# Kernel tuning notes

Hardware: AMD Instinct MI355X
Metric: run time of the kernel (lower is better)

The kernel has to match this reference:

```python
import jax, jax.numpy as jnp
import numpy as np

EPS = 1e-12

def gcn_layer(x, W, row, col, vals, n_nodes):
    # support = x @ W ; out = relu(spmm(adj, support)) with adj in COO form
    support = x @ W                                  # [N, out]
    msgs = vals[:, None] * support[col]              # [E, out] gather
    agg = jax.ops.segment_sum(msgs, row, num_segments=n_nodes)
    return jax.nn.relu(agg)

def l2norm(x):
    return x / jnp.maximum(jnp.linalg.norm(x, axis=1, keepdims=True), EPS)

def setup_inputs() -> dict:
    key = jax.random.key(0)
    ks = jax.random.split(key, 16)
    N, D, A, Da, E = 20000, 1000, 1000, 100, 160000
    inp = {
        'emb_sr': jax.random.normal(ks[0], (N, D), jnp.float32) * 0.02,
        'emb_tg': jax.random.normal(ks[1], (N, D), jnp.float32) * 0.02,
        'attr_weight_sr': jax.random.uniform(ks[2], (N, A), jnp.float32),
        'attr_weight_tg': jax.random.uniform(ks[3], (N, A), jnp.float32),
        'row_sr': jax.random.randint(ks[4], (E,), 0, N, jnp.int32),
        'col_sr': jax.random.randint(ks[5], (E,), 0, N, jnp.int32),
        'vals_sr': jax.random.uniform(ks[6], (E,), jnp.float32),
        'row_tg': jax.random.randint(ks[7], (E,), 0, N, jnp.int32),
        'col_tg': jax.random.randint(ks[8], (E,), 0, N, jnp.int32),
        'vals_tg': jax.random.uniform(ks[9], (E,), jnp.float32),
        'W_s0': jax.random.normal(ks[10], (D, D), jnp.float32) * (1.0 / np.sqrt(D)),
        'W_s1': jax.random.normal(ks[11], (D, D), jnp.float32) * (1.0 / np.sqrt(D)),
        'W_a11': jax.random.normal(ks[12], (A, Da), jnp.float32) * (1.0 / np.sqrt(A)),
        'W_a12': jax.random.normal(ks[13], (A, Da), jnp.float32) * (1.0 / np.sqrt(A)),
        'W_a2': jax.random.normal(ks[14], (Da, Da), jnp.float32) * (1.0 / np.sqrt(Da)),
    }
    return inp

def reference(emb_sr, emb_tg, attr_weight_sr, attr_weight_tg,
              row_sr, col_sr, vals_sr, row_tg, col_tg, vals_tg,
              W_s0, W_s1, W_a11, W_a12, W_a2):
    N = emb_sr.shape[0]
    M = emb_tg.shape[0]
    # structural branch: 2 shared GCN layers over each graph
    sr = emb_sr
    tg = emb_tg
    for W in (W_s0, W_s1):
        sr = gcn_layer(sr, W, row_sr, col_sr, vals_sr, N)
        tg = gcn_layer(tg, W, row_tg, col_tg, vals_tg, M)
    sr = l2norm(sr)
    tg = l2norm(tg)
    # attribute branch
    sr_a = gcn_layer(attr_weight_sr, W_a11, row_sr, col_sr, vals_sr, N)
    sr_a = gcn_layer(sr_a, W_a2, row_sr, col_sr, vals_sr, N)
    tg_a = gcn_layer(attr_weight_tg, W_a12, row_tg, col_tg, vals_tg, M)
    tg_a = gcn_layer(tg_a, W_a2, row_tg, col_tg, vals_tg, M)
    return (sr, tg, sr_a, tg_a)
```

## Files before the change

kernel.cpp:

```cpp
#include <hip/hip_runtime.h>

#define N_NODES 20000
#define D_IN    1000
#define E_EDGES 160000
#define DA      100

#define MP   20096
#define DP   1024
#define DAP  128
#define MBLK 157
#define NRB  1250
#define PEMAX (E_EDGES + 4 * N_NODES)

typedef __bf16 bf16x8 __attribute__((ext_vector_type(8)));
typedef float  f32x4  __attribute__((ext_vector_type(4)));
typedef short  short8v __attribute__((ext_vector_type(8)));

__device__ __forceinline__ short f2bf(float f) {
  __bf16 h = (__bf16)f;
  return *(short*)&h;
}
__device__ __forceinline__ float bf2f(short s) {
  return __uint_as_float(((unsigned)(unsigned short)s) << 16);
}

#define GLDS16(g, l) __builtin_amdgcn_global_load_lds( \
    (const __attribute__((address_space(1))) void*)(g), \
    (__attribute__((address_space(3))) void*)(l), 16, 0, 0)


__global__ void cvt_pad2_k(const float* __restrict__ s0, const float* __restrict__ s1,
                           int R, int C,
                           short* __restrict__ d0, short* __restrict__ d1, int Cp) {
  const float* src = blockIdx.z ? s1 : s0;
  short* dst = blockIdx.z ? d1 : d0;
  int r = blockIdx.y;
  int c0 = threadIdx.x * 4;
  short4 o = {0, 0, 0, 0};
  if (r < R) {
    if (c0 + 3 < C) {
      float4 v = *(const float4*)&src[(size_t)r * C + c0];
      o.x = f2bf(v.x); o.y = f2bf(v.y); o.z = f2bf(v.z); o.w = f2bf(v.w);
    } else {
#pragma unroll
      for (int j = 0; j < 4; ++j) {
        float v = (c0 + j < C) ? src[(size_t)r * C + c0 + j] : 0.f;
        ((short*)&o)[j] = f2bf(v);
      }
    }
  }
  *(short4*)&dst[(size_t)r * Cp + c0] = o;
}

__global__ void cvt_w_t2_k(const float* __restrict__ s0, const float* __restrict__ s1,
                           int K, int Nc,
                           short* __restrict__ d0, short* __restrict__ d1, int Kp) {
  const float* src = blockIdx.z ? s1 : s0;
  short* dst = blockIdx.z ? d1 : d0;
  int n = blockIdx.y;
  int k = blockIdx.x * blockDim.x + threadIdx.x;
  if (k >= Kp) return;
  float v = (k < K && n < Nc) ? src[(size_t)k * Nc + n] : 0.f;
  dst[(size_t)n * Kp + k] = f2bf(v);
}

__global__ void zero_int_k(int* p, int n) {
  int i = blockIdx.x * blockDim.x + threadIdx.x;
  if (i < n) p[i] = 0;
}


__global__ void hist2_k(const int* __restrict__ row0, const int* __restrict__ row1, int E,
                        int* __restrict__ deg0, int* __restrict__ deg1) {
  int e = blockIdx.x * blockDim.x + threadIdx.x;
  if (e < E) atomicAdd(&deg0[row0[e]], 1);
  else if (e < 2 * E) atomicAdd(&deg1[row1[e - E]], 1);
}

#define SCAN_T 1024
#define SCAN_C 20
__launch_bounds__(SCAN_T)
__global__ void scan_pad2_k(const int* __restrict__ dg0, const int* __restrict__ dg1, int n,
                            int* __restrict__ p0, int* __restrict__ p1) {
  const int* deg = blockIdx.x ? dg1 : dg0;
  int* poffs = blockIdx.x ? p1 : p0;
  __shared__ int lds[SCAN_T];
  int t = threadIdx.x;
  int base = t * SCAN_C;
  int v[SCAN_C];
  int s = 0;
#pragma unroll
  for (int i = 0; i < SCAN_C; ++i) {
    int idx = base + i;
    int x = (idx < n) ? ((deg[idx] + 3) & ~3) : 0;
    s += x;
    v[i] = s;
  }
  lds[t] = s;
  __syncthreads();
  for (int off = 1; off < SCAN_T; off <<= 1) {
    int add = (t >= off) ? lds[t - off] : 0;
    __syncthreads();
    lds[t] += add;
    __syncthreads();
  }
  int prefix = lds[t] - s;
#pragma unroll
  for (int i = 0; i < SCAN_C; ++i) {
    int idx = base + i;
    if (idx < n) poffs[idx + 1] = v[i] + prefix;
  }
  if (t == 0) poffs[0] = 0;
}

__global__ void scatter_pack2_k(const int* __restrict__ row0, const int* __restrict__ col0,
                                const float* __restrict__ val0,
                                const int* __restrict__ row1, const int* __restrict__ col1,
                                const float* __restrict__ val1, int E,
                                const int* __restrict__ po0, const int* __restrict__ po1,
                                int* __restrict__ cur0, int* __restrict__ cur1,
                                int2* __restrict__ pk0, int2* __restrict__ pk1) {
  int e = blockIdx.x * blockDim.x + threadIdx.x;
  if (e < E) {
    int r = row0[e];
    int p = atomicAdd(&cur0[r], 1);
    pk0[po0[r] + p] = make_int2(col0[e], __float_as_int(val0[e]));
  } else if (e < 2 * E) {
    int ee = e - E;
    int r = row1[ee];
    int p = atomicAdd(&cur1[r], 1);
    pk1[po1[r] + p] = make_int2(col1[ee], __float_as_int(val1[ee]));
  }
}

__launch_bounds__(256, 2)
__global__ void gemm_bf16_k(const short* __restrict__ A0, const short* __restrict__ A1, int lda,
                            const short* __restrict__ Bt0, const short* __restrict__ Bt1, int ldb,
                            short* __restrict__ C0, short* __restrict__ C1, int ldc, int K,
                            int nbCol, int nbRow) {
  __shared__ short As[128 * 64];
  __shared__ short Bs[128 * 64];

  int orig = blockIdx.x;
  int nwg = gridDim.x;
  int q = nwg >> 3, rr = nwg & 7;
  int xcd = orig & 7, idx = orig >> 3;
  int wg = (xcd < rr ? xcd * (q + 1) : rr * (q + 1) + (xcd - rr) * q) + idx;
  int colB = wg % nbCol;
  int t2   = wg / nbCol;
  int rowB = t2 % nbRow;
  int z    = t2 / nbRow;

  const short* A  = z ? A1 : A0;
  const short* Bt = z ? Bt1 : Bt0;
  short* C        = z ? C1 : C0;

  const int tid  = threadIdx.x;
  const int lane = tid & 63;
  const int wid  = tid >> 6;
  const int wr   = wid >> 1;
  const int wc   = wid & 1;
  const int rowBase = rowB * 128;
  const int colBase = colB * 128;

  const int lrow = lane >> 3;
  const int kofs = (lane & 7) * 8;

  f32x4 acc[4][4];
#pragma unroll
  for (int m = 0; m < 4; ++m)
#pragma unroll
    for (int n = 0; n < 4; ++n)
      acc[m][n] = (f32x4){0.f, 0.f, 0.f, 0.f};

  for (int k0 = 0; k0 < K; k0 += 64) {
#pragma unroll
    for (int c = 0; c < 4; ++c) {
      int chunk = wid * 4 + c;
      int r = chunk * 8 + lrow;
      const short* g = A + (size_t)(rowBase + r) * lda + k0 + kofs;
      GLDS16(g, &As[chunk * 8 * 64]);
    }
#pragma unroll
    for (int c = 0; c < 4; ++c) {
      int chunk = wid * 4 + c;
      int r = chunk * 8 + lrow;
      const short* g = Bt + (size_t)(colBase + r) * ldb + k0 + kofs;
      GLDS16(g, &Bs[chunk * 8 * 64]);
    }
    __syncthreads();

    bf16x8 af[2][4], bfr[2][4];
#pragma unroll
    for (int kk = 0; kk < 2; ++kk) {
#pragma unroll
      for (int i = 0; i < 4; ++i) {
        int ar = wr * 64 + i * 16 + (lane & 15);
        af[kk][i]  = *(const bf16x8*)&As[ar * 64 + kk * 32 + (lane >> 4) * 8];
        int br = wc * 64 + i * 16 + (lane & 15);
        bfr[kk][i] = *(const bf16x8*)&Bs[br * 64 + kk * 32 + (lane >> 4) * 8];
      }
    }
#pragma unroll
    for (int kk = 0; kk < 2; ++kk)
#pragma unroll
      for (int m = 0; m < 4; ++m)
#pragma unroll
        for (int n = 0; n < 4; ++n)
          acc[m][n] = __builtin_amdgcn_mfma_f32_16x16x32_bf16(
              af[kk][m], bfr[kk][n], acc[m][n], 0, 0, 0);
    __syncthreads();
  }

#pragma unroll
  for (int m = 0; m < 4; ++m) {
#pragma unroll
    for (int n = 0; n < 4; ++n) {
      int row0 = rowBase + wr * 64 + m * 16 + (lane >> 4) * 4;
      int col  = colBase + wc * 64 + n * 16 + (lane & 15);
#pragma unroll
      for (int reg = 0; reg < 4; ++reg)
        C[(size_t)(row0 + reg) * ldc + col] = f2bf(acc[m][n][reg]);
    }
  }
}

template<int NCHUNK, int MODE>
__launch_bounds__(256)
__global__ void spmm_v5(const int* __restrict__ po0, const int* __restrict__ po1,
                        const int2* __restrict__ pk0, const int2* __restrict__ pk1,
                        const short* __restrict__ S0, const short* __restrict__ S1, int ldS,
                        short* __restrict__ oB0, short* __restrict__ oB1, int ldB,
                        float* __restrict__ oF0, float* __restrict__ oF1, int outCols) {
  int orig = blockIdx.x;
  int chunk, graph, rowBlk;
  if (NCHUNK == 8) {
    chunk = orig & 7;
    int idx = orig >> 3;
    graph = idx / NRB;
    rowBlk = idx - graph * NRB;
  } else {
    chunk = 0;
    graph = orig / NRB;
    rowBlk = orig - graph * NRB;
  }
  const int* poffs   = graph ? po1 : po0;
  const int2* packed = graph ? pk1 : pk0;
  const short* S     = graph ? S1 : S0;
  short* outB        = graph ? oB1 : oB0;
  float* outF        = graph ? oF1 : oF0;

  const int lane16 = threadIdx.x & 15;
  const int rowloc = threadIdx.x >> 4;
  const int r  = rowBlk * 16 + rowloc;
  const int c0 = chunk * 128 + lane16 * 8;

  int e0 = poffs[r], e1 = poffs[r + 1];
  float acc[8];
#pragma unroll
  for (int j = 0; j < 8; ++j) acc[j] = 0.f;

  for (int i = e0; i < e1; i += 4) {
    const int4* p4 = (const int4*)&packed[i];
    int4 a = p4[0];
    int4 b = p4[1];
    short8v s0 = *(const short8v*)&S[(size_t)a.x * ldS + c0];
    short8v s1 = *(const short8v*)&S[(size_t)a.z * ldS + c0];
    short8v s2 = *(const short8v*)&S[(size_t)b.x * ldS + c0];
    short8v s3 = *(const short8v*)&S[(size_t)b.z * ldS + c0];
    float v0 = __int_as_float(a.y);
    float v1 = __int_as_float(a.w);
    float v2 = __int_as_float(b.y);
    float v3 = __int_as_float(b.w);
#pragma unroll
    for (int j = 0; j < 8; ++j) {
      acc[j] += v0 * bf2f(s0[j]);
      acc[j] += v1 * bf2f(s1[j]);
      acc[j] += v2 * bf2f(s2[j]);
      acc[j] += v3 * bf2f(s3[j]);
    }
  }
#pragma unroll
  for (int j = 0; j < 8; ++j) acc[j] = fmaxf(acc[j], 0.f);

  if (MODE == 0) {
    short8v o;
#pragma unroll
    for (int j = 0; j < 8; ++j) o[j] = f2bf(acc[j]);
    *(short8v*)&outB[(size_t)r * ldB + c0] = o;
  } else {
#pragma unroll
    for (int j = 0; j < 8; ++j)
      if (c0 + j < outCols)
        outF[(size_t)r * outCols + c0 + j] = acc[j];
  }
}

__global__ void l2norm2_k(const short* __restrict__ H0, const short* __restrict__ H1, int ldH,
                          float* __restrict__ o0, float* __restrict__ o1, int cols) {
  const short* H = blockIdx.y ? H1 : H0;
  float* out = blockIdx.y ? o1 : o0;
  __shared__ float red[4];
  int r = blockIdx.x;
  int t = threadIdx.x;
  float s = 0.f;
  for (int c = t; c < ldH; c += 256) {
    float v = bf2f(H[(size_t)r * ldH + c]);
    s += v * v;
  }
  for (int off = 32; off >= 1; off >>= 1) s += __shfl_down(s, off, 64);
  if ((t & 63) == 0) red[t >> 6] = s;
  __syncthreads();
  float tot = red[0] + red[1] + red[2] + red[3];
  float inv = 1.f / fmaxf(sqrtf(tot), 1e-12f);
  for (int c = t; c < cols; c += 256)
    out[(size_t)r * cols + c] = bf2f(H[(size_t)r * ldH + c]) * inv;
}


extern "C" void kernel_launch(void* const* d_in, const int* in_sizes, int n_in,
                              void* d_out, int out_size, void* d_ws, size_t ws_size,
                              hipStream_t stream) {
  const float* emb_sr  = (const float*)d_in[0];
  const float* emb_tg  = (const float*)d_in[1];
  const float* attr_sr = (const float*)d_in[2];
  const float* attr_tg = (const float*)d_in[3];
  const int*   row_sr  = (const int*)d_in[4];
  const int*   col_sr  = (const int*)d_in[5];
  const float* vals_sr = (const float*)d_in[6];
  const int*   row_tg  = (const int*)d_in[7];
  const int*   col_tg  = (const int*)d_in[8];
  const float* vals_tg = (const float*)d_in[9];
  const float* W_s0    = (const float*)d_in[10];
  const float* W_s1    = (const float*)d_in[11];
  const float* W_a11   = (const float*)d_in[12];
  const float* W_a12   = (const float*)d_in[13];
  const float* W_a2    = (const float*)d_in[14];

  const int N = N_NODES, Dd = D_IN, E = E_EDGES;

  char* ws = (char*)d_ws;
  size_t off = 0;
  auto alloc = [&](size_t bytes) -> void* {
    void* p = ws + off;
    off += (bytes + 255) & ~(size_t)255;
    return p;
  };
  short* X0 = (short*)alloc((size_t)MP * DP * 2);
  short* X1 = (short*)alloc((size_t)MP * DP * 2);
  short* T0 = (short*)alloc((size_t)MP * DP * 2);
  short* T1 = (short*)alloc((size_t)MP * DP * 2);
  short* Ws0t  = (short*)alloc((size_t)DP * DP * 2);
  short* Ws1t  = (short*)alloc((size_t)DP * DP * 2);
  short* Wa11t = (short*)alloc((size_t)DAP * DP * 2);
  short* Wa12t = (short*)alloc((size_t)DAP * DP * 2);
  short* Wa2t  = (short*)alloc((size_t)DAP * DAP * 2);
  int*  ibuf    = (int*)alloc((size_t)4 * N * 4);
  int2* pack_sr = (int2*)alloc((size_t)PEMAX * 8);
  int2* pack_tg = (int2*)alloc((size_t)PEMAX * 8);
  int*  poffs_sr = (int*)alloc((size_t)(N + 1) * 4);
  int*  poffs_tg = (int*)alloc((size_t)(N + 1) * 4);
  if (off > ws_size) return;

  int* deg_sr = ibuf;
  int* cur_sr = ibuf + N;
  int* deg_tg = ibuf + 2 * N;
  int* cur_tg = ibuf + 3 * N;
  const int ZERO_N = 4 * N + 2 * (PEMAX * 2);

  float* out_sr  = (float*)d_out;
  float* out_tg  = out_sr + (size_t)N * Dd;
  float* out_sra = out_tg + (size_t)N * Dd;
  float* out_tga = out_sra + (size_t)N * DA;

  zero_int_k<<<dim3((ZERO_N + 255) / 256), 256, 0, stream>>>(ibuf, ZERO_N);
  hist2_k<<<dim3((2 * E + 255) / 256), 256, 0, stream>>>(row_sr, row_tg, E, deg_sr, deg_tg);
  scan_pad2_k<<<2, SCAN_T, 0, stream>>>(deg_sr, deg_tg, N, poffs_sr, poffs_tg);
  scatter_pack2_k<<<dim3((2 * E + 255) / 256), 256, 0, stream>>>(
      row_sr, col_sr, vals_sr, row_tg, col_tg, vals_tg, E,
      poffs_sr, poffs_tg, cur_sr, cur_tg, pack_sr, pack_tg);

  cvt_w_t2_k<<<dim3(DP / 256, DP, 2), 256, 0, stream>>>(W_s0, W_s1, Dd, Dd, Ws0t, Ws1t, DP);
  cvt_w_t2_k<<<dim3(DP / 256, DAP, 2), 256, 0, stream>>>(W_a11, W_a12, Dd, DA, Wa11t, Wa12t, DP);
  cvt_w_t2_k<<<dim3(1, DAP, 1), 256, 0, stream>>>(W_a2, W_a2, DA, DA, Wa2t, Wa2t, DAP);

  cvt_pad2_k<<<dim3(1, MP, 2), 256, 0, stream>>>(emb_sr, emb_tg, N, Dd, X0, X1, DP);
  gemm_bf16_k<<<dim3(8 * MBLK * 2), 256, 0, stream>>>(X0, X1, DP, Ws0t, Ws0t, DP,
                                                      T0, T1, DP, DP, 8, MBLK);
  spmm_v5<8, 0><<<dim3(8 * 2 * NRB), 256, 0, stream>>>(
      poffs_sr, poffs_tg, pack_sr, pack_tg, T0, T1, DP, X0, X1, DP, nullptr, nullptr, 0);
  gemm_bf16_k<<<dim3(8 * MBLK * 2), 256, 0, stream>>>(X0, X1, DP, Ws1t, Ws1t, DP,
                                                      T0, T1, DP, DP, 8, MBLK);
  spmm_v5<8, 0><<<dim3(8 * 2 * NRB), 256, 0, stream>>>(
      poffs_sr, poffs_tg, pack_sr, pack_tg, T0, T1, DP, X0, X1, DP, nullptr, nullptr, 0);
  l2norm2_k<<<dim3(N, 2), 256, 0, stream>>>(X0, X1, DP, out_sr, out_tg, Dd);

  cvt_pad2_k<<<dim3(1, MP, 2), 256, 0, stream>>>(attr_sr, attr_tg, N, Dd, X0, X1, DP);
  gemm_bf16_k<<<dim3(1 * MBLK * 2), 256, 0, stream>>>(X0, X1, DP, Wa11t, Wa12t, DP,
                                                      T0, T1, DAP, DP, 1, MBLK);
  spmm_v5<1, 0><<<dim3(2 * NRB), 256, 0, stream>>>(
      poffs_sr, poffs_tg, pack_sr, pack_tg, T0, T1, DAP, X0, X1, DAP, nullptr, nullptr, 0);
  gemm_bf16_k<<<dim3(1 * MBLK * 2), 256, 0, stream>>>(X0, X1, DAP, Wa2t, Wa2t, DAP,
                                                      T0, T1, DAP, DAP, 1, MBLK);
  spmm_v5<1, 1><<<dim3(2 * NRB), 256, 0, stream>>>(
      poffs_sr, poffs_tg, pack_sr, pack_tg, T0, T1, DAP, nullptr, nullptr, 0, out_sra, out_tga, DA);
}
```

Measured before the change: 636.2 us.

## Add 4-stage pipelined 128x256 bf16 GEMM for structural layers

Introduces a new GEMM kernel with 512 threads, 128x256 output tiles, and a four-buffer LDS ring. It uses direct global-to-LDS loads issued three k-steps ahead, with waitcnt-based synchronization and MFMA priority raising. It replaces the older 128x128 GEMM for the two large 1024-wide structural layers. The goal is to hide global memory latency and raise tile reuse, at the cost of more LDS, one block per CU, and hand-tuned waitcnt counts that must match the load count.

```diff
diff --git a/kernel.cpp b/kernel.cpp
--- a/kernel.cpp
+++ b/kernel.cpp
@@ -130,6 +130,119 @@
     int r = row1[ee];
     int p = atomicAdd(&cur1[r], 1);
     pk1[po1[r] + p] = make_int2(col1[ee], __float_as_int(val1[ee]));
+  }
+}
+
+template<int NT>
+__launch_bounds__(512, 1)
+__global__ void gemm_pipe_k(const short* __restrict__ A0, const short* __restrict__ A1, int lda,
+                            const short* __restrict__ Bt0, const short* __restrict__ Bt1, int ldb,
+                            short* __restrict__ C0, short* __restrict__ C1, int ldc,
+                            int nbCol, int nbRow) {
+  __shared__ short As[4][128 * 32];
+  __shared__ short Bs[4][256 * 32];
+
+  int orig = blockIdx.x;
+  int nwg = gridDim.x;
+  int q = nwg >> 3, rr = nwg & 7;
+  int xcd = orig & 7, idx = orig >> 3;
+  int wg = (xcd < rr ? xcd * (q + 1) : rr * (q + 1) + (xcd - rr) * q) + idx;
+  int colB = wg % nbCol;
+  int t2 = wg / nbCol;
+  int rowB = t2 % nbRow;
+  int z = t2 / nbRow;
+
+  const short* A  = z ? A1 : A0;
+  const short* Bt = z ? Bt1 : Bt0;
+  short* C        = z ? C1 : C0;
+
+  const int tid  = threadIdx.x;
+  const int lane = tid & 63;
+  const int wid  = tid >> 6;
+  const int wm   = wid >> 2;
+  const int wn   = wid & 3;
+  const int rowBase = rowB * 128;
+  const int colBase = colB * 256;
+
+  const int sRow   = tid >> 2;
+  const int sChunk = (tid & 3) ^ ((tid >> 3) & 3);
+  const short* gA  = A  + (size_t)(rowBase + sRow) * lda + sChunk * 8;
+  const short* gB0 = Bt + (size_t)(colBase + sRow) * ldb + sChunk * 8;
+  const short* gB1 = Bt + (size_t)(colBase + 128 + sRow) * ldb + sChunk * 8;
+  const int ldsA  = wid * 512;
+  const int ldsB0 = wid * 512;
+  const int ldsB1 = 4096 + wid * 512;
+
+  int rA[4], rB[4];
+#pragma unroll
+  for (int m = 0; m < 4; ++m) {
+    int row = wm * 64 + m * 16 + (lane & 15);
+    int ch = (lane >> 4) ^ ((row >> 1) & 3);
+    rA[m] = row * 32 + ch * 8;
+  }
+#pragma unroll
+  for (int n = 0; n < 4; ++n) {
+    int row = wn * 64 + n * 16 + (lane & 15);
+    int ch = (lane >> 4) ^ ((row >> 1) & 3);
+    rB[n] = row * 32 + ch * 8;
+  }
+
+  f32x4 acc[4][4];
+#pragma unroll
+  for (int m = 0; m < 4; ++m)
+#pragma unroll
+    for (int n = 0; n < 4; ++n)
+      acc[m][n] = (f32x4){0.f, 0.f, 0.f, 0.f};
+
+#define STAGE_T(kt, b) do { \
+    GLDS16(gA  + (kt) * 32, &As[b][ldsA]);  \
+    GLDS16(gB0 + (kt) * 32, &Bs[b][ldsB0]); \
+    GLDS16(gB1 + (kt) * 32, &Bs[b][ldsB1]); \
+  } while (0)
+
+  STAGE_T(0, 0);
+  STAGE_T(1, 1);
+  STAGE_T(2, 2);
+  asm volatile("s_waitcnt vmcnt(6)" ::: "memory");
+  __builtin_amdgcn_s_barrier();
+  __builtin_amdgcn_sched_barrier(0);
+
+  for (int t = 0; t < NT; ++t) {
+    const int buf = t & 3;
+    const short* pa = &As[buf][0];
+    const short* pb = &Bs[buf][0];
+    bf16x8 af[4], bfr[4];
+#pragma unroll
+    for (int m = 0; m < 4; ++m) af[m] = *(const bf16x8*)&pa[rA[m]];
+#pragma unroll
+    for (int n = 0; n < 4; ++n) bfr[n] = *(const bf16x8*)&pb[rB[n]];
+    if (t + 3 < NT) STAGE_T(t + 3, (t + 3) & 3);
+    __builtin_amdgcn_s_barrier();
+    __builtin_amdgcn_s_setprio(1);
+#pragma unroll
+    for (int m = 0; m < 4; ++m)
+#pragma unroll
+      for (int n = 0; n < 4; ++n)
+        acc[m][n] = __builtin_amdgcn_mfma_f32_16x16x32_bf16(af[m], bfr[n], acc[m][n], 0, 0, 0);
+    __builtin_amdgcn_s_setprio(0);
+    if (t < NT - 3)       { asm volatile("s_waitcnt vmcnt(6)" ::: "memory"); }
+    else if (t == NT - 3) { asm volatile("s_waitcnt vmcnt(3)" ::: "memory"); }
+    else if (t == NT - 2) { asm volatile("s_waitcnt vmcnt(0)" ::: "memory"); }
+    __builtin_amdgcn_s_barrier();
+    __builtin_amdgcn_sched_barrier(0);
+  }
+#undef STAGE_T
+
+#pragma unroll
+  for (int m = 0; m < 4; ++m) {
+#pragma unroll
+    for (int n = 0; n < 4; ++n) {
+      int r0 = rowBase + wm * 64 + m * 16 + (lane >> 4) * 4;
+      int c  = colBase + wn * 64 + n * 16 + (lane & 15);
+#pragma unroll
+      for (int reg = 0; reg < 4; ++reg)
+        C[(size_t)(r0 + reg) * ldc + c] = f2bf(acc[m][n][reg]);
+    }
   }
 }
 
@@ -385,12 +498,12 @@
   cvt_w_t2_k<<<dim3(1, DAP, 1), 256, 0, stream>>>(W_a2, W_a2, DA, DA, Wa2t, Wa2t, DAP);
 
   cvt_pad2_k<<<dim3(1, MP, 2), 256, 0, stream>>>(emb_sr, emb_tg, N, Dd, X0, X1, DP);
-  gemm_bf16_k<<<dim3(8 * MBLK * 2), 256, 0, stream>>>(X0, X1, DP, Ws0t, Ws0t, DP,
-                                                      T0, T1, DP, DP, 8, MBLK);
+  gemm_pipe_k<32><<<dim3(MBLK * 4 * 2), 512, 0, stream>>>(X0, X1, DP, Ws0t, Ws0t, DP,
+                                                          T0, T1, DP, 4, MBLK);
   spmm_v5<8, 0><<<dim3(8 * 2 * NRB), 256, 0, stream>>>(
       poffs_sr, poffs_tg, pack_sr, pack_tg, T0, T1, DP, X0, X1, DP, nullptr, nullptr, 0);
-  gemm_bf16_k<<<dim3(8 * MBLK * 2), 256, 0, stream>>>(X0, X1, DP, Ws1t, Ws1t, DP,
-                                                      T0, T1, DP, DP, 8, MBLK);
+  gemm_pipe_k<32><<<dim3(MBLK * 4 * 2), 512, 0, stream>>>(X0, X1, DP, Ws1t, Ws1t, DP,
+                                                          T0, T1, DP, 4, MBLK);
   spmm_v5<8, 0><<<dim3(8 * 2 * NRB), 256, 0, stream>>>(
       poffs_sr, poffs_tg, pack_sr, pack_tg, T0, T1, DP, X0, X1, DP, nullptr, nullptr, 0);
   l2norm2_k<<<dim3(N, 2), 256, 0, stream>>>(X0, X1, DP, out_sr, out_tg, Dd);
```

Result: slower. 656.8 us (+3.2%).

## Replace big structural GEMMs with 256x256-tile 8-wave pipelined bf16 MFMA kernel

Applied to the files above, without the earlier changes.

Adds a new GEMM kernel for the two 1024-wide structural layers. It uses 256x256 output tiles, 512 threads and an 8-slot LDS ring filled by direct global-to-LDS loads, with explicit vmcnt waits, barriers and setprio around the MFMA bursts. Row padding grows from 20096 to 20224 so rows are a multiple of 256. The aim is more data reuse per tile and overlap of loads with MFMA work, at the cost of one block per CU and a fragile hand-written wait schedule.

```diff
diff --git a/kernel.cpp b/kernel.cpp
--- a/kernel.cpp
+++ b/kernel.cpp
@@ -5,7 +5,7 @@
 #define E_EDGES 160000
 #define DA      100
 
-#define MP   20096
+#define MPAD 20224
 #define DP   1024
 #define DAP  128
 #define MBLK 157
@@ -130,6 +130,117 @@
     int r = row1[ee];
     int p = atomicAdd(&cur1[r], 1);
     pk1[po1[r] + p] = make_int2(col1[ee], __float_as_int(val1[ee]));
+  }
+}
+
+__launch_bounds__(512, 1)
+__global__ void gemm8p_k(const short* __restrict__ A0, const short* __restrict__ A1, int lda,
+                         const short* __restrict__ Bt0, const short* __restrict__ Bt1, int ldb,
+                         short* __restrict__ C0, short* __restrict__ C1, int ldc,
+                         int nbCol, int nbRow) {
+  __shared__ short lds[8][8192];
+
+  int orig = blockIdx.x;
+  int nwg = gridDim.x;
+  int q = nwg >> 3, rr = nwg & 7;
+  int xcd = orig & 7, idx = orig >> 3;
+  int wg = (xcd < rr ? xcd * (q + 1) : rr * (q + 1) + (xcd - rr) * q) + idx;
+  int colB = wg % nbCol;
+  int t2 = wg / nbCol;
+  int rowB = t2 % nbRow;
+  int z = t2 / nbRow;
+
+  const short* A  = z ? A1 : A0;
+  const short* Bt = z ? Bt1 : Bt0;
+  short* C        = z ? C1 : C0;
+
+  const int tid  = threadIdx.x;
+  const int lane = tid & 63;
+  const int wid  = tid >> 6;
+  const int wm   = wid >> 2;
+  const int wn   = wid & 3;
+  const int rowBase = rowB * 256;
+  const int colBase = colB * 256;
+
+  const int sC = (lane & 3) ^ ((lane >> 3) & 3);
+  const short* baseA = A  + (size_t)(rowBase + wid * 32 + (lane >> 2)) * lda + sC * 8;
+  const short* baseB = Bt + (size_t)(colBase + wid * 32 + (lane >> 2)) * ldb + sC * 8;
+
+  const int chunkR = (lane >> 4) ^ ((lane >> 1) & 3);
+  const int offA = (wm * 128 + (lane & 15)) * 32 + chunkR * 8;
+  const int offB = (wn * 64  + (lane & 15)) * 32 + chunkR * 8;
+
+  f32x4 acc[8][4];
+#pragma unroll
+  for (int m = 0; m < 8; ++m)
+#pragma unroll
+    for (int n = 0; n < 4; ++n)
+      acc[m][n] = (f32x4){0.f, 0.f, 0.f, 0.f};
+
+#define STAGE_HALF(h) do { \
+    int tt_ = (h) >> 2; \
+    int kc_ = tt_ * 64 + (((h) >> 1) & 1) * 32; \
+    short* dst_ = &lds[(h) & 7][wid * 1024]; \
+    if ((h) & 1) { GLDS16(baseB + kc_, dst_); GLDS16(baseB + kc_ + 16 * ldb, dst_ + 512); } \
+    else         { GLDS16(baseA + kc_, dst_); GLDS16(baseA + kc_ + 16 * lda, dst_ + 512); } \
+  } while (0)
+
+  STAGE_HALF(0); STAGE_HALF(1); STAGE_HALF(2); STAGE_HALF(3); STAGE_HALF(4);
+  asm volatile("s_waitcnt vmcnt(6)" ::: "memory");
+  __builtin_amdgcn_s_barrier();
+  __builtin_amdgcn_sched_barrier(0);
+
+#define PHASE(P, KS, QM) do { \
+    const int sA_ = (4 * t + 2 * (KS)) & 7; \
+    const short* pA_ = &lds[sA_][0]; \
+    const short* pB_ = &lds[sA_ + 1][0]; \
+    bf16x8 af_[4], bv_[4]; \
+    _Pragma("unroll") \
+    for (int m = 0; m < 4; ++m) af_[m] = *(const bf16x8*)&pA_[offA + ((QM) * 4 + m) * 512]; \
+    _Pragma("unroll") \
+    for (int n = 0; n < 4; ++n) bv_[n] = *(const bf16x8*)&pB_[offB + n * 512]; \
+    { int h_ = 4 * t + (P) + 5; \
+      if (h_ < 64) STAGE_HALF(h_); } \
+    __builtin_amdgcn_s_barrier(); \
+    __builtin_amdgcn_s_setprio(1); \
+    _Pragma("unroll") \
+    for (int m = 0; m < 4; ++m) \
+      _Pragma("unroll") \
+      for (int n = 0; n < 4; ++n) \
+        acc[(QM) * 4 + m][n] = __builtin_amdgcn_mfma_f32_16x16x32_bf16( \
+            af_[m], bv_[n], acc[(QM) * 4 + m][n], 0, 0, 0); \
+    __builtin_amdgcn_s_setprio(0); \
+    if (t < 14)      { asm volatile("s_waitcnt vmcnt(6)" ::: "memory"); } \
+    else if (t == 14) { \
+      if ((P) < 3)   { asm volatile("s_waitcnt vmcnt(6)" ::: "memory"); } \
+      else           { asm volatile("s_waitcnt vmcnt(4)" ::: "memory"); } \
+    } else { \
+      if ((P) == 0)  { asm volatile("s_waitcnt vmcnt(2)" ::: "memory"); } \
+      else           { asm volatile("s_waitcnt vmcnt(0)" ::: "memory"); } \
+    } \
+    __builtin_amdgcn_s_barrier(); \
+    __builtin_amdgcn_sched_barrier(0); \
+  } while (0)
+
+  for (int t = 0; t < 16; ++t) {
+    PHASE(0, 0, 0);
+    PHASE(1, 0, 1);
+    PHASE(2, 1, 0);
+    PHASE(3, 1, 1);
+  }
+#undef PHASE
+#undef STAGE_HALF
+
+#pragma unroll
+  for (int gm = 0; gm < 8; ++gm) {
+#pragma unroll
+    for (int n = 0; n < 4; ++n) {
+      int r0 = rowBase + wm * 128 + gm * 16 + (lane >> 4) * 4;
+      int c  = colBase + wn * 64 + n * 16 + (lane & 15);
+#pragma unroll
+      for (int reg = 0; reg < 4; ++reg)
+        C[(size_t)(r0 + reg) * ldc + c] = f2bf(acc[gm][n][reg]);
+    }
   }
 }
 
@@ -346,10 +457,10 @@
     off += (bytes + 255) & ~(size_t)255;
     return p;
   };
-  short* X0 = (short*)alloc((size_t)MP * DP * 2);
-  short* X1 = (short*)alloc((size_t)MP * DP * 2);
-  short* T0 = (short*)alloc((size_t)MP * DP * 2);
-  short* T1 = (short*)alloc((size_t)MP * DP * 2);
+  short* X0 = (short*)alloc((size_t)MPAD * DP * 2);
+  short* X1 = (short*)alloc((size_t)MPAD * DP * 2);
+  short* T0 = (short*)alloc((size_t)MPAD * DP * 2);
+  short* T1 = (short*)alloc((size_t)MPAD * DP * 2);
   short* Ws0t  = (short*)alloc((size_t)DP * DP * 2);
   short* Ws1t  = (short*)alloc((size_t)DP * DP * 2);
   short* Wa11t = (short*)alloc((size_t)DAP * DP * 2);
@@ -384,18 +495,18 @@
   cvt_w_t2_k<<<dim3(DP / 256, DAP, 2), 256, 0, stream>>>(W_a11, W_a12, Dd, DA, Wa11t, Wa12t, DP);
   cvt_w_t2_k<<<dim3(1, DAP, 1), 256, 0, stream>>>(W_a2, W_a2, DA, DA, Wa2t, Wa2t, DAP);
 
-  cvt_pad2_k<<<dim3(1, MP, 2), 256, 0, stream>>>(emb_sr, emb_tg, N, Dd, X0, X1, DP);
-  gemm_bf16_k<<<dim3(8 * MBLK * 2), 256, 0, stream>>>(X0, X1, DP, Ws0t, Ws0t, DP,
-                                                      T0, T1, DP, DP, 8, MBLK);
+  cvt_pad2_k<<<dim3(1, MPAD, 2), 256, 0, stream>>>(emb_sr, emb_tg, N, Dd, X0, X1, DP);
+  gemm8p_k<<<dim3(79 * 4 * 2), 512, 0, stream>>>(X0, X1, DP, Ws0t, Ws0t, DP,
+                                                 T0, T1, DP, 4, 79);
   spmm_v5<8, 0><<<dim3(8 * 2 * NRB), 256, 0, stream>>>(
       poffs_sr, poffs_tg, pack_sr, pack_tg, T0, T1, DP, X0, X1, DP, nullptr, nullptr, 0);
-  gemm_bf16_k<<<dim3(8 * MBLK * 2), 256, 0, stream>>>(X0, X1, DP, Ws1t, Ws1t, DP,
-                                                      T0, T1, DP, DP, 8, MBLK);
+  gemm8p_k<<<dim3(79 * 4 * 2), 512, 0, stream>>>(X0, X1, DP, Ws1t, Ws1t, DP,
+                                                 T0, T1, DP, 4, 79);
   spmm_v5<8, 0><<<dim3(8 * 2 * NRB), 256, 0, stream>>>(
       poffs_sr, poffs_tg, pack_sr, pack_tg, T0, T1, DP, X0, X1, DP, nullptr, nullptr, 0);
   l2norm2_k<<<dim3(N, 2), 256, 0, stream>>>(X0, X1, DP, out_sr, out_tg, Dd);
 
-  cvt_pad2_k<<<dim3(1, MP, 2), 256, 0, stream>>>(attr_sr, attr_tg, N, Dd, X0, X1, DP);
+  cvt_pad2_k<<<dim3(1, MPAD, 2), 256, 0, stream>>>(attr_sr, attr_tg, N, Dd, X0, X1, DP);
   gemm_bf16_k<<<dim3(1 * MBLK * 2), 256, 0, stream>>>(X0, X1, DP, Wa11t, Wa12t, DP,
                                                       T0, T1, DAP, DP, 1, MBLK);
   spmm_v5<1, 0><<<dim3(2 * NRB), 256, 0, stream>>>(
```

After: 636.9 us. Within noise of the previous version (+0.1%).
